# Kernel optimization log

Measured on AMD Instinct MI355X. Metric: run time of the kernel, lower is better.

## Reference

```python
import jax, jax.numpy as jnp
import numpy as np

EPS = 1e-12

def _l2norm(v):
    # torch.nn.functional.normalize(p=2) with eps clamp
    return v / jnp.maximum(jnp.linalg.norm(v), EPS)

def _spectral_weight(W, U):
    # W: (out, in) flattened 1x1 conv weight; U: (1, out) power-iteration buffer.
    # One power iteration, all under stop_gradient (torch.no_grad in original).
    V = _l2norm(U @ W)            # (1, in)
    Unew = _l2norm(V @ W.T)       # (1, out)
    sigma = (Unew @ W @ V.T)[0, 0]
    return W / jax.lax.stop_gradient(sigma)

def _conv1x1(x, W, b):
    # x: (b,c,h,w), W: (o,c), b: (o,)
    return jnp.einsum('oc,bchw->bohw', W, x) + b[None, :, None, None]

def setup_inputs() -> dict:
    key = jax.random.key(0)
    ks = jax.random.split(key, 11)
    B, C, H, W = 4, 256, 64, 64
    Ck = C // 8
    return {
        'x':   jax.random.normal(ks[0], (B, C, H, W), jnp.float32),
        'f_w': jax.random.normal(ks[1], (Ck, C), jnp.float32) * 0.05,
        'f_b': jax.random.normal(ks[2], (Ck,), jnp.float32) * 0.05,
        'f_u': jax.random.uniform(ks[3], (1, Ck), jnp.float32),
        'g_w': jax.random.normal(ks[4], (Ck, C), jnp.float32) * 0.05,
        'g_b': jax.random.normal(ks[5], (Ck,), jnp.float32) * 0.05,
        'g_u': jax.random.uniform(ks[6], (1, Ck), jnp.float32),
        'h_w': jax.random.normal(ks[7], (C, C), jnp.float32) * 0.05,
        'h_b': jax.random.normal(ks[8], (C,), jnp.float32) * 0.05,
        'h_u': jax.random.uniform(ks[9], (1, C), jnp.float32),
        'gamma': jax.random.normal(ks[10], (1, 1), jnp.float32),
    }

def reference(x, f_w, f_b, f_u, g_w, g_b, g_u, h_w, h_b, h_u, gamma):
    b, c, h, w = x.shape
    hw = h * w
    key_ = _conv1x1(x, _spectral_weight(f_w, f_u), f_b).reshape(b, -1, hw).transpose(0, 2, 1)  # (b,hw,ck)
    query = _conv1x1(x, _spectral_weight(g_w, g_u), g_b).reshape(b, -1, hw)                    # (b,ck,hw)
    attn = jax.nn.softmax(jnp.einsum('bnd,bdm->bnm', key_, query), axis=-1)                    # (b,hw,hw)
    value = _conv1x1(x, _spectral_weight(h_w, h_u), h_b).reshape(b, -1, hw)                    # (b,c,hw)
    out = jnp.einsum('bnm,bcm->bnc', attn, value)                                              # (b,hw,c)
    # Faithful to original: raw view of (b,hw,c) contiguous buffer into (b,c,h,w)
    out = out.reshape(b, c, h, w)
    return gamma[0, 0] * out + x
```

## Files before the change

kernel.cpp:

```cpp
#include <hip/hip_runtime.h>


constexpr int kC   = 256;
constexpr int kHW  = 4096;
constexpr int kB   = 4;
constexpr int kCHW = kC * kHW;

typedef short bf16x8 __attribute__((ext_vector_type(8)));
typedef float f32x4  __attribute__((ext_vector_type(4)));
typedef unsigned short u16;

#if __has_builtin(__builtin_amdgcn_exp2f)
#define EXP2(x) __builtin_amdgcn_exp2f(x)
#else
#define EXP2(x) exp2f(x)
#endif

__device__ __forceinline__ u16 f2bf(float f) {
    union { float f; unsigned u; } v; v.f = f;
    unsigned u = v.u;
    return (u16)((u + 0x7fffu + ((u >> 16) & 1u)) >> 16);
}
__device__ __forceinline__ float bf2f(u16 h) {
    union { unsigned u; float f; } v; v.u = ((unsigned)h) << 16;
    return v.f;
}

__global__ __launch_bounds__(1024) void k_sigma(
    const float* __restrict__ fw, const float* __restrict__ fu,
    const float* __restrict__ gw, const float* __restrict__ gu,
    const float* __restrict__ hww, const float* __restrict__ hu,
    float* __restrict__ sig, u16* __restrict__ wh, u16* __restrict__ wl)
{
    const int which = blockIdx.x;
    const float* W = which == 0 ? fw : (which == 1 ? gw : hww);
    const float* U = which == 0 ? fu : (which == 1 ? gu : hu);
    const int O = (which == 2) ? 256 : 32;
    const int t = threadIdx.x;

    __shared__ float par[4][256];
    __shared__ float red[256];
    __shared__ __align__(16) float Vv[256];

    {
        const int i = t & 255, och = t >> 8;
        int olim = O - och * 64; olim = olim < 0 ? 0 : (olim > 64 ? 64 : olim);
        float p = 0.f;
        for (int oo = 0; oo < olim; ++oo) {
            const int o = och * 64 + oo;
            p += U[o] * W[o * 256 + i];
        }
        par[och][i] = p;
    }
    __syncthreads();
    float t1 = 0.f;
    if (t < 256) {
        t1 = par[0][t] + par[1][t] + par[2][t] + par[3][t];
        red[t] = t1 * t1;
    }
    __syncthreads();
    for (int s = 128; s > 0; s >>= 1) { if (t < s) red[t] += red[t + s]; __syncthreads(); }
    if (t < 256) Vv[t] = t1 / fmaxf(sqrtf(red[0]), 1e-12f);
    __syncthreads();

    {
        const int o = t & 255, ich = t >> 8;
        float q = 0.f;
        if (o < O) {
            const float4* Wr = (const float4*)(W + (size_t)o * 256 + ich * 64);
            const float4* Vr = (const float4*)(&Vv[ich * 64]);
#pragma unroll
            for (int j = 0; j < 16; ++j) {
                const float4 w = Wr[j]; const float4 v = Vr[j];
                q += w.x * v.x + w.y * v.y + w.z * v.z + w.w * v.w;
            }
        }
        par[ich][o] = q;
    }
    __syncthreads();
    if (t < 256) {
        const float t2 = par[0][t] + par[1][t] + par[2][t] + par[3][t];
        red[t] = t2 * t2;
    }
    __syncthreads();
    for (int s = 128; s > 0; s >>= 1) { if (t < s) red[t] += red[t + s]; __syncthreads(); }
    if (t == 0) {
        const float s2 = red[0];
        sig[which] = fmaxf(sqrtf(s2), 1e-12f) / s2;
    }

    const int nElem = O * 256;
    const int gbase = (which == 0) ? 0 : (which == 1 ? 32 : 64);
    for (int i = t; i < nElem; i += 1024) {
        const int o = i >> 8, ci = i & 255;
        const int g = gbase + o;
        const int idx = ((g >> 4) * 8 + (ci >> 5)) * 512 + (g & 15) * 32 + (ci & 31);
        const float f = W[i];
        const u16 h = f2bf(f);
        wh[idx] = h;
        wl[idx] = f2bf(f - bf2f(h));
    }
}

__global__ __launch_bounds__(512) void k_proj(
    const float* __restrict__ x,
    const u16* __restrict__ wh, const u16* __restrict__ wl,
    const float* __restrict__ fb, const float* __restrict__ gb,
    const float* __restrict__ hb, const float* __restrict__ sig,
    u16* __restrict__ Kc, u16* __restrict__ Qc, u16* __restrict__ Vb)
{
    __shared__ __align__(16) float xs[256][64];
    __shared__ float bLDS[320];

    const int t = threadIdx.x;
    const int wave = t >> 6, lane = t & 63;
    const int quad = lane >> 4, l15 = lane & 15;
    const int b = blockIdx.y;
    const int n0 = blockIdx.x * 64;
    const int nch = wave & 3, cohalf = wave >> 2;

    constexpr float kLog2e = 1.44269504f;

    {
        const int r4i = lane >> 4, c16 = lane & 15;
        const float* xg = x + (size_t)b * kCHW + (size_t)r4i * kHW + n0 + c16 * 4;
#pragma unroll
        for (int j = 0; j < 8; ++j) {
            const int cibase = (wave * 8 + j) * 4;
            __builtin_amdgcn_global_load_lds(
                (const __attribute__((address_space(1))) void*)(xg + (size_t)cibase * kHW),
                (__attribute__((address_space(3))) void*)&xs[cibase][0], 16, 0, 0);
        }
    }
    if (t < 320) bLDS[t] = (t < 32) ? fb[t]
                         : (t < 64) ? gb[t - 32] * kLog2e
                         : hb[t - 64];
    __syncthreads();

    const int n = nch * 16 + l15;
    bf16x8 bh[8], bl[8];
#pragma unroll
    for (int s = 0; s < 8; ++s) {
        union { u16 a[8]; bf16x8 v; } H, L;
#pragma unroll
        for (int j = 0; j < 8; ++j) {
            const float v = xs[s * 32 + quad * 8 + j][n];
            const u16 h = f2bf(v);
            H.a[j] = h; L.a[j] = f2bf(v - bf2f(h));
        }
        bh[s] = H.v; bl[s] = L.v;
    }

    const u16* whp = wh + l15 * 32 + quad * 8;
    const u16* wlp = wl + l15 * 32 + quad * 8;

    f32x4 acc[10] = {};
#pragma unroll
    for (int c = 0; c < 10; ++c) {
        const size_t base = (size_t)(cohalf * 10 + c) * 4096;
#pragma unroll
        for (int s = 0; s < 8; ++s) {
            const bf16x8 ah = *(const bf16x8*)(whp + base + s * 512);
            const bf16x8 al = *(const bf16x8*)(wlp + base + s * 512);
            acc[c] = __builtin_amdgcn_mfma_f32_16x16x32_bf16(ah, bh[s], acc[c], 0, 0, 0);
            acc[c] = __builtin_amdgcn_mfma_f32_16x16x32_bf16(ah, bl[s], acc[c], 0, 0, 0);
            acc[c] = __builtin_amdgcn_mfma_f32_16x16x32_bf16(al, bh[s], acc[c], 0, 0, 0);
        }
    }

    const float s0 = sig[0], s1 = sig[1] * kLog2e, s2 = sig[2];
#pragma unroll
    for (int c = 0; c < 10; ++c) {
        const int cog0 = (cohalf * 10 + c) * 16;
        const float inv = (cog0 < 32) ? s0 : (cog0 < 64) ? s1 : s2;
#pragma unroll
        for (int r = 0; r < 4; ++r) {
            const int co = cog0 + quad * 4 + r;
            const float v = acc[c][r] * inv + bLDS[co];
            if (co < 64) {
                u16* H = (co < 32) ? Kc : Qc;
                const int d = co & 31;
                const u16 h = f2bf(v);
                const u16 l = f2bf(v - bf2f(h));
                const size_t off = (size_t)(b * kHW + n0 + n) * 64;
                H[off + d] = h;
                H[off + 32 + d] = l;
            } else {
                Vb[((size_t)b * kC + (co - 64)) * kHW + n0 + n] = f2bf(v);
            }
        }
    }
}

__global__ __launch_bounds__(512, 4) void k_attn(
    const u16* __restrict__ Kc, const u16* __restrict__ Qc,
    const u16* __restrict__ Vb,
    u16* __restrict__ Op, float* __restrict__ Sl, int mtiles)
{
    __shared__ __align__(16) u16 Qt[2][4096];
    __shared__ __align__(16) u16 Pt[2][4096];
    __shared__ float lsum[8][16];

    const int t = threadIdx.x;
    const int wave = t >> 6, lane = t & 63;
    const int quad = lane >> 4, l15 = lane & 15;
    const int sg = wave >> 1, half = wave & 1;

    const int id = blockIdx.x;
    const int xcd = id & 7;
    const int b = xcd >> 1;
    const int nb0 = ((xcd & 1) * 32 + ((id >> 3) & 31)) * 64;
    const int mh = id >> 8;
    const int mt0 = mh * mtiles, mt1 = mt0 + mtiles;

    const u16* Kb  = Kc + (size_t)b * kHW * 64;
    const u16* Qb  = Qc + (size_t)b * kHW * 64;
    const u16* Vbb = Vb + (size_t)b * kC * kHW;

    const size_t krow = (size_t)(nb0 + sg * 16 + l15) * 64 + (size_t)quad * 8;
    const bf16x8 kh = *(const bf16x8*)(Kb + krow);
    const bf16x8 kl = *(const bf16x8*)(Kb + krow + 32);

    const u16* vrow[2];
#pragma unroll
    for (int ct = 0; ct < 2; ++ct)
        vrow[ct] = Vbb + (size_t)(wave * 32 + ct * 16 + l15) * kHW + quad * 8;

    const int qs_row = lane >> 3, qs_ch = lane & 7;
    const int rloc = wave * 8 + qs_row;
    const int qswz = (qs_ch ^ (rloc & 7)) << 3;

    f32x4 O[8] = {};
    float lrow = 0.f;
    bf16x8 vc[4], vn[4];

    __builtin_amdgcn_global_load_lds(
        (const __attribute__((address_space(1))) void*)
            (Qb + (size_t)(mt0 * 64 + rloc) * 64 + qswz),
        (__attribute__((address_space(3))) void*)&Qt[0][wave * 512], 16, 0, 0);
#pragma unroll
    for (int ct = 0; ct < 2; ++ct)
#pragma unroll
        for (int ks = 0; ks < 2; ++ks)
            vc[ct * 2 + ks] = *(const bf16x8*)(vrow[ct] + mt0 * 64 + ks * 32);
    __syncthreads();

    for (int mt = mt0; mt < mt1; ++mt) {
        const int cur = mt & 1;
        const int m0 = mt * 64;

        if (mt < mt1 - 1) {
            __builtin_amdgcn_global_load_lds(
                (const __attribute__((address_space(1))) void*)
                    (Qb + (size_t)(m0 + 64 + rloc) * 64 + qswz),
                (__attribute__((address_space(3))) void*)&Qt[cur ^ 1][wave * 512], 16, 0, 0);
        }
        const int m0v = (mt < mt1 - 1) ? m0 + 64 : m0;
#pragma unroll
        for (int ct = 0; ct < 2; ++ct)
#pragma unroll
            for (int ks = 0; ks < 2; ++ks)
                vn[ct * 2 + ks] = *(const bf16x8*)(vrow[ct] + m0v + ks * 32);

        f32x4 s[2];
#pragma unroll
        for (int mi2 = 0; mi2 < 2; ++mi2) {
            const int mi = half * 2 + mi2;
            const int rbase = (mi * 16 + l15) * 64;
            const bf16x8 qhv = *(const bf16x8*)&Qt[cur][rbase + ((quad       ^ (l15 & 7)) << 3)];
            const bf16x8 qlv = *(const bf16x8*)&Qt[cur][rbase + (((quad + 4) ^ (l15 & 7)) << 3)];
            f32x4 a = { 0.f, 0.f, 0.f, 0.f };
            a = __builtin_amdgcn_mfma_f32_16x16x32_bf16(qhv, kl, a, 0, 0, 0);
            a = __builtin_amdgcn_mfma_f32_16x16x32_bf16(qlv, kh, a, 0, 0, 0);
            a = __builtin_amdgcn_mfma_f32_16x16x32_bf16(qhv, kh, a, 0, 0, 0);
            s[mi2] = a;
        }

        {
            const int prow = sg * 16 + l15;
#pragma unroll
            for (int mi2 = 0; mi2 < 2; ++mi2) {
                const float p0 = EXP2(s[mi2][0]);
                const float p1 = EXP2(s[mi2][1]);
                const float p2 = EXP2(s[mi2][2]);
                const float p3 = EXP2(s[mi2][3]);
                lrow += (p0 + p1) + (p2 + p3);
                const unsigned d0 = __builtin_amdgcn_perm(
                    __float_as_uint(p1), __float_as_uint(p0), 0x07060302u);
                const unsigned d1 = __builtin_amdgcn_perm(
                    __float_as_uint(p3), __float_as_uint(p2), 0x07060302u);
                const int mi = half * 2 + mi2;
                const int chunk = 2 * mi + (quad >> 1);
                const int off = prow * 64 + ((chunk ^ (l15 & 7)) << 3) + (quad & 1) * 4;
                *(uint2*)(Pt[cur] + off) = make_uint2(d0, d1);
            }
        }

        __syncthreads();

#pragma unroll
        for (int ks = 0; ks < 2; ++ks) {
#pragma unroll
            for (int rg = 0; rg < 4; ++rg) {
                const bf16x8 pa = *(const bf16x8*)&Pt[cur][(rg * 16 + l15) * 64
                                     + (((ks * 4 + quad) ^ (l15 & 7)) << 3)];
#pragma unroll
                for (int ct = 0; ct < 2; ++ct)
                    O[rg * 2 + ct] = __builtin_amdgcn_mfma_f32_16x16x32_bf16(
                        pa, vc[ct * 2 + ks], O[rg * 2 + ct], 0, 0, 0);
            }
        }

#pragma unroll
        for (int i = 0; i < 4; ++i) vc[i] = vn[i];
    }

    lrow += __shfl_xor(lrow, 16);
    lrow += __shfl_xor(lrow, 32);
    if (lane < 16) lsum[wave][l15] = lrow;
    __syncthreads();
    if (half == 0 && lane < 16)
        Sl[(size_t)(mh * 4 + b) * kHW + nb0 + sg * 16 + l15]
            = lsum[wave][l15] + lsum[wave ^ 1][l15];

    u16* Opb = Op + (size_t)(mh * 4 + b) * kHW * 256;
#pragma unroll
    for (int rg = 0; rg < 4; ++rg) {
#pragma unroll
        for (int ct = 0; ct < 2; ++ct) {
#pragma unroll
            for (int r = 0; r < 4; ++r) {
                const int nn = nb0 + rg * 16 + quad * 4 + r;
                const int c = wave * 32 + ct * 16 + l15;
                Opb[(size_t)nn * 256 + c] = f2bf(O[rg * 2 + ct][r]);
            }
        }
    }
}

template <int NS>
__global__ __launch_bounds__(256) void k_merge(
    const float* __restrict__ x, const float* __restrict__ gamma,
    const u16* __restrict__ Op, const float* __restrict__ Sl,
    float* __restrict__ out)
{
    const int tid = blockIdx.x * 256 + threadIdx.x;
    const int cg = tid & 31;
    const int n  = (tid >> 5) & 4095;
    const int b  = tid >> 17;
    const int c0 = cg * 8;

    float l = 0.f;
#pragma unroll
    for (int s = 0; s < NS; ++s) l += Sl[(size_t)(s * 4 + b) * kHW + n];
    const float invL = 1.f / l;
    const float g = gamma[0];

    const size_t base = ((size_t)b * kHW + n) * 256 + c0;

    float o[8] = {};
#pragma unroll
    for (int s = 0; s < NS; ++s) {
        const uint4 A = *(const uint4*)(Op + base + (size_t)s * 4 * kHW * 256);
        const unsigned aw[4] = { A.x, A.y, A.z, A.w };
#pragma unroll
        for (int j = 0; j < 8; ++j)
            o[j] += bf2f((u16)(aw[j >> 1] >> ((j & 1) * 16)));
    }

    const float4 x0 = *(const float4*)(x + base);
    const float4 x1 = *(const float4*)(x + base + 4);
    float4 r0, r1;
    r0.x = g * o[0] * invL + x0.x; r0.y = g * o[1] * invL + x0.y;
    r0.z = g * o[2] * invL + x0.z; r0.w = g * o[3] * invL + x0.w;
    r1.x = g * o[4] * invL + x1.x; r1.y = g * o[5] * invL + x1.y;
    r1.z = g * o[6] * invL + x1.z; r1.w = g * o[7] * invL + x1.w;
    *(float4*)(out + base)     = r0;
    *(float4*)(out + base + 4) = r1;
}

extern "C" void kernel_launch(void* const* d_in, const int* in_sizes, int n_in,
                              void* d_out, int out_size, void* d_ws, size_t ws_size,
                              hipStream_t stream)
{
    const float* x     = (const float*)d_in[0];
    const float* fw    = (const float*)d_in[1];
    const float* fb    = (const float*)d_in[2];
    const float* fu    = (const float*)d_in[3];
    const float* gw    = (const float*)d_in[4];
    const float* gb    = (const float*)d_in[5];
    const float* gu    = (const float*)d_in[6];
    const float* hww   = (const float*)d_in[7];
    const float* hb    = (const float*)d_in[8];
    const float* hu    = (const float*)d_in[9];
    const float* gamma = (const float*)d_in[10];
    float* out = (float*)d_out;

    char* ws = (char*)d_ws;
    float* sig = (float*)ws;
    u16* wh = (u16*)(ws + 1024);
    u16* wl = wh + 320 * 256;
    u16* Kc = (u16*)(ws + (512u << 10));
    u16* Qc = (u16*)(ws + (2560u << 10));
    u16* Vb = (u16*)(ws + (4608u << 10));
    char* opBase = ws + (12800u << 10);

    const size_t need4 = (12800u << 10) + 4ull * 8 * 1024 * 1024 + (256u << 10);
    const int ns = (ws_size >= need4) ? 4 : 2;
    const int mtiles = 64 / ns;

    u16* Op = (u16*)opBase;
    float* Sl = (float*)(opBase + (size_t)ns * 8 * 1024 * 1024);

    k_sigma<<<dim3(3), dim3(1024), 0, stream>>>(fw, fu, gw, gu, hww, hu, sig, wh, wl);
    k_proj<<<dim3(64, 4), dim3(512), 0, stream>>>(x, wh, wl, fb, gb, hb, sig,
                                                  Kc, Qc, Vb);
    k_attn<<<dim3(256 * ns), dim3(512), 0, stream>>>(Kc, Qc, Vb, Op, Sl, mtiles);
    if (ns == 4)
        k_merge<4><<<dim3(2048), dim3(256), 0, stream>>>(x, gamma, Op, Sl, out);
    else
        k_merge<2><<<dim3(2048), dim3(256), 0, stream>>>(x, gamma, Op, Sl, out);
}
```

Before: 254.2 us.

## Halve attention block rows to 32 with 4 waves covering 64 channels each

Attention blocks now handle 32 query rows with 256 threads instead of 64 rows with 512 threads, and each wave accumulates 64 output channels instead of 32. The number of blocks per split doubles, and the key split is fixed at 2 instead of choosing 4 when the workspace allows. The intent is to raise the MFMA count per P fragment load, cut LDS space per block, and reduce partial-output traffic in the merge. In exchange, each thread holds twice as many V register fragments, which could lower occupancy, and K/Q tiles are loaded by more blocks.

```diff
diff --git a/kernel.cpp b/kernel.cpp
--- a/kernel.cpp
+++ b/kernel.cpp
@@ -192,14 +192,14 @@
     }
 }
 
-__global__ __launch_bounds__(512, 4) void k_attn(
+__global__ __launch_bounds__(256, 4) void k_attn(
     const u16* __restrict__ Kc, const u16* __restrict__ Qc,
     const u16* __restrict__ Vb,
     u16* __restrict__ Op, float* __restrict__ Sl, int mtiles)
 {
     __shared__ __align__(16) u16 Qt[2][4096];
-    __shared__ __align__(16) u16 Pt[2][4096];
-    __shared__ float lsum[8][16];
+    __shared__ __align__(16) u16 Pt[2][2048];
+    __shared__ float lsum[4][16];
 
     const int t = threadIdx.x;
     const int wave = t >> 6, lane = t & 63;
@@ -209,8 +209,9 @@
     const int id = blockIdx.x;
     const int xcd = id & 7;
     const int b = xcd >> 1;
-    const int nb0 = ((xcd & 1) * 32 + ((id >> 3) & 31)) * 64;
-    const int mh = id >> 8;
+    const int rb = (id >> 3) & 63;
+    const int nb0 = ((xcd & 1) * 64 + rb) * 32;
+    const int mh = id >> 9;
     const int mt0 = mh * mtiles, mt1 = mt0 + mtiles;
 
     const u16* Kb  = Kc + (size_t)b * kHW * 64;
@@ -221,25 +222,31 @@
     const bf16x8 kh = *(const bf16x8*)(Kb + krow);
     const bf16x8 kl = *(const bf16x8*)(Kb + krow + 32);
 
-    const u16* vrow[2];
-#pragma unroll
-    for (int ct = 0; ct < 2; ++ct)
-        vrow[ct] = Vbb + (size_t)(wave * 32 + ct * 16 + l15) * kHW + quad * 8;
+    const u16* vrow[4];
+#pragma unroll
+    for (int ct = 0; ct < 4; ++ct)
+        vrow[ct] = Vbb + (size_t)(wave * 64 + ct * 16 + l15) * kHW + quad * 8;
 
     const int qs_row = lane >> 3, qs_ch = lane & 7;
-    const int rloc = wave * 8 + qs_row;
-    const int qswz = (qs_ch ^ (rloc & 7)) << 3;
+    const int rloc0 = wave * 8 + qs_row;
+    const int rloc1 = rloc0 + 32;
+    const int qswz0 = (qs_ch ^ (rloc0 & 7)) << 3;
+    const int qswz1 = (qs_ch ^ (rloc1 & 7)) << 3;
 
     f32x4 O[8] = {};
     float lrow = 0.f;
-    bf16x8 vc[4], vn[4];
+    bf16x8 vc[8], vn[8];
 
     __builtin_amdgcn_global_load_lds(
         (const __attribute__((address_space(1))) void*)
-            (Qb + (size_t)(mt0 * 64 + rloc) * 64 + qswz),
+            (Qb + (size_t)(mt0 * 64 + rloc0) * 64 + qswz0),
         (__attribute__((address_space(3))) void*)&Qt[0][wave * 512], 16, 0, 0);
-#pragma unroll
-    for (int ct = 0; ct < 2; ++ct)
+    __builtin_amdgcn_global_load_lds(
+        (const __attribute__((address_space(1))) void*)
+            (Qb + (size_t)(mt0 * 64 + rloc1) * 64 + qswz1),
+        (__attribute__((address_space(3))) void*)&Qt[0][wave * 512 + 2048], 16, 0, 0);
+#pragma unroll
+    for (int ct = 0; ct < 4; ++ct)
 #pragma unroll
         for (int ks = 0; ks < 2; ++ks)
             vc[ct * 2 + ks] = *(const bf16x8*)(vrow[ct] + mt0 * 64 + ks * 32);
@@ -252,12 +259,16 @@
         if (mt < mt1 - 1) {
             __builtin_amdgcn_global_load_lds(
                 (const __attribute__((address_space(1))) void*)
-                    (Qb + (size_t)(m0 + 64 + rloc) * 64 + qswz),
+                    (Qb + (size_t)(m0 + 64 + rloc0) * 64 + qswz0),
                 (__attribute__((address_space(3))) void*)&Qt[cur ^ 1][wave * 512], 16, 0, 0);
+            __builtin_amdgcn_global_load_lds(
+                (const __attribute__((address_space(1))) void*)
+                    (Qb + (size_t)(m0 + 64 + rloc1) * 64 + qswz1),
+                (__attribute__((address_space(3))) void*)&Qt[cur ^ 1][wave * 512 + 2048], 16, 0, 0);
         }
         const int m0v = (mt < mt1 - 1) ? m0 + 64 : m0;
 #pragma unroll
-        for (int ct = 0; ct < 2; ++ct)
+        for (int ct = 0; ct < 4; ++ct)
 #pragma unroll
             for (int ks = 0; ks < 2; ++ks)
                 vn[ct * 2 + ks] = *(const bf16x8*)(vrow[ct] + m0v + ks * 32);
@@ -301,18 +312,18 @@
 #pragma unroll
         for (int ks = 0; ks < 2; ++ks) {
 #pragma unroll
-            for (int rg = 0; rg < 4; ++rg) {
+            for (int rg = 0; rg < 2; ++rg) {
                 const bf16x8 pa = *(const bf16x8*)&Pt[cur][(rg * 16 + l15) * 64
                                      + (((ks * 4 + quad) ^ (l15 & 7)) << 3)];
 #pragma unroll
-                for (int ct = 0; ct < 2; ++ct)
-                    O[rg * 2 + ct] = __builtin_amdgcn_mfma_f32_16x16x32_bf16(
-                        pa, vc[ct * 2 + ks], O[rg * 2 + ct], 0, 0, 0);
+                for (int ct = 0; ct < 4; ++ct)
+                    O[rg * 4 + ct] = __builtin_amdgcn_mfma_f32_16x16x32_bf16(
+                        pa, vc[ct * 2 + ks], O[rg * 4 + ct], 0, 0, 0);
             }
         }
 
 #pragma unroll
-        for (int i = 0; i < 4; ++i) vc[i] = vn[i];
+        for (int i = 0; i < 8; ++i) vc[i] = vn[i];
     }
 
     lrow += __shfl_xor(lrow, 16);
@@ -325,14 +336,14 @@
 
     u16* Opb = Op + (size_t)(mh * 4 + b) * kHW * 256;
 #pragma unroll
-    for (int rg = 0; rg < 4; ++rg) {
-#pragma unroll
-        for (int ct = 0; ct < 2; ++ct) {
+    for (int rg = 0; rg < 2; ++rg) {
+#pragma unroll
+        for (int ct = 0; ct < 4; ++ct) {
 #pragma unroll
             for (int r = 0; r < 4; ++r) {
                 const int nn = nb0 + rg * 16 + quad * 4 + r;
-                const int c = wave * 32 + ct * 16 + l15;
-                Opb[(size_t)nn * 256 + c] = f2bf(O[rg * 2 + ct][r]);
+                const int c = wave * 64 + ct * 16 + l15;
+                Opb[(size_t)nn * 256 + c] = f2bf(O[rg * 4 + ct][r]);
             }
         }
     }
@@ -403,21 +414,12 @@
     u16* Kc = (u16*)(ws + (512u << 10));
     u16* Qc = (u16*)(ws + (2560u << 10));
     u16* Vb = (u16*)(ws + (4608u << 10));
-    char* opBase = ws + (12800u << 10);
-
-    const size_t need4 = (12800u << 10) + 4ull * 8 * 1024 * 1024 + (256u << 10);
-    const int ns = (ws_size >= need4) ? 4 : 2;
-    const int mtiles = 64 / ns;
-
-    u16* Op = (u16*)opBase;
-    float* Sl = (float*)(opBase + (size_t)ns * 8 * 1024 * 1024);
+    u16* Op = (u16*)(ws + (12800u << 10));
+    float* Sl = (float*)(ws + (12800u << 10) + 2ull * 8 * 1024 * 1024);
 
     k_sigma<<<dim3(3), dim3(1024), 0, stream>>>(fw, fu, gw, gu, hww, hu, sig, wh, wl);
     k_proj<<<dim3(64, 4), dim3(512), 0, stream>>>(x, wh, wl, fb, gb, hb, sig,
                                                   Kc, Qc, Vb);
-    k_attn<<<dim3(256 * ns), dim3(512), 0, stream>>>(Kc, Qc, Vb, Op, Sl, mtiles);
-    if (ns == 4)
-        k_merge<4><<<dim3(2048), dim3(256), 0, stream>>>(x, gamma, Op, Sl, out);
-    else
-        k_merge<2><<<dim3(2048), dim3(256), 0, stream>>>(x, gamma, Op, Sl, out);
-}
+    k_attn<<<dim3(1024), dim3(256), 0, stream>>>(Kc, Qc, Vb, Op, Sl, 32);
+    k_merge<2><<<dim3(2048), dim3(256), 0, stream>>>(x, gamma, Op, Sl, out);
+}
```

After: 333.9 us. 31.4% more time.
